# Optimization experiments

Measured on AMD Instinct MI355X. Metric: run time of the kernel, lower is better.

## Reference

```python
import jax, jax.numpy as jnp
import numpy as np

DIM = 256
HEADS = 8
DIM_HEAD = 64
INNER = HEADS * DIM_HEAD           # 512
DPG = DIM // HEADS                 # 32 in-channels per group (grouped conv)
EPS = 1e-5


def setup_inputs() -> dict:
    key = jax.random.key(0)
    ks = jax.random.split(key, 7)
    b, p, k = 4, 1024, 32
    x = jax.random.normal(ks[0], (b, p, k, DIM), dtype=jnp.float32)
    # BatchNorm2d affine params (torch default init: gamma=1, beta=0)
    bn_gamma = jnp.ones((DIM,), jnp.float32)
    bn_beta = jnp.zeros((DIM,), jnp.float32)
    # grouped 1x1 conv weights: per head maps DPG -> DIM_HEAD, shape [H, DIM_HEAD, DPG]
    Wq = jax.random.normal(ks[1], (HEADS, DIM_HEAD, DPG), jnp.float32) * 0.02
    Wk = jax.random.normal(ks[2], (HEADS, DIM_HEAD, DPG), jnp.float32) * 0.02
    Wv = jax.random.normal(ks[3], (HEADS, DIM_HEAD, DPG), jnp.float32) * 0.02
    # output Linear: y = x @ Wout + bout, Wout [INNER, DIM]
    Wout = jax.random.normal(ks[4], (INNER, DIM), jnp.float32) * 0.02
    bout = jnp.zeros((DIM,), jnp.float32)
    return {"x": x, "bn_gamma": bn_gamma, "bn_beta": bn_beta,
            "Wq": Wq, "Wk": Wk, "Wv": Wv, "Wout": Wout, "bout": bout}


def reference(x, bn_gamma, bn_beta, Wq, Wk, Wv, Wout, bout):
    b, p, k, d = x.shape
    scale = DIM_HEAD ** (-0.5)
    # BatchNorm2d in training mode: per-channel batch stats over (b, p, k)
    mean = jnp.mean(x, axis=(0, 1, 2))
    var = jnp.var(x, axis=(0, 1, 2))           # biased variance (torch BN normalization)
    xn = (x - mean) * jax.lax.rsqrt(var + EPS) * bn_gamma + bn_beta
    # grouped 1x1 conv projections: split channels into HEADS groups of DPG
    xg = xn.reshape(b, p, k, HEADS, DPG)       # [b,p,k,h,c]
    q = jnp.einsum('bpkhc,hoc->bphko', xg, Wq)  # [b,p,h,k,dim_head]
    kk = jnp.einsum('bpkhc,hoc->bphko', xg, Wk)
    v = jnp.einsum('bpkhc,hoc->bphko', xg, Wv)
    # attention over neighbors within each point
    dots = jnp.einsum('bphid,bphjd->bphij', q, kk) * scale  # [b,p,h,k,k]
    attn = jax.nn.softmax(dots, axis=-1)
    out = jnp.einsum('bphij,bphjd->bphid', attn, v)         # [b,p,h,k,dim_head]
    out = out.transpose(0, 1, 3, 2, 4).reshape(b, p, k, INNER)  # b p k (h d)
    return out @ Wout + bout                   # [b,p,k,dim]
```

## Files before the change

### kernel.cpp

```cpp
#include <hip/hip_runtime.h>

#define DIM    256
#define HEADS  8
#define DH     64
#define DPG    32
#define KNB    32
#define INNER  512
#define EPS    1e-5f

#define WS_SUM  0
#define WS_SSQ  256
#define WS_SC   512
#define WS_SH   768
#define WS_WF   1024
#define WS_QB   25600
#define WS_WT   27136

typedef float f32x4  __attribute__((ext_vector_type(4)));
typedef short bf16x8 __attribute__((ext_vector_type(8)));

__device__ __forceinline__ unsigned short f2bf(float f){
    unsigned u = __float_as_uint(f);
    u += 0x7fffu + ((u >> 16) & 1u);
    return (unsigned short)(u >> 16);
}
__device__ __forceinline__ unsigned packbf(float a, float b){
    return (unsigned)f2bf(a) | ((unsigned)f2bf(b) << 16);
}
__device__ __forceinline__ bf16x8 pack8(f32x4 a, f32x4 b){
    union { unsigned u[4]; bf16x8 v; } r;
    r.u[0] = packbf(a[0], a[1]); r.u[1] = packbf(a[2], a[3]);
    r.u[2] = packbf(b[0], b[1]); r.u[3] = packbf(b[2], b[3]);
    return r.v;
}

#define QKSWZ(row, col) ((row) * 64 + ((col) ^ ((((row) ^ ((row) >> 3)) & 7) << 3)))
#define VTSWZ(row, col) ((row) * 32 + ((col) ^ (((row) & 3) << 3)))

__global__ __launch_bounds__(256) void bn_stats_k(const f32x4* __restrict__ x4,
                                                  float* __restrict__ ws, int n4) {
    __shared__ f32x4 rs[4][64], rss[4][64];
    int tid = blockIdx.x * 256 + threadIdx.x;
    int stride = gridDim.x * 256;
    f32x4 s  = {0.f, 0.f, 0.f, 0.f};
    f32x4 ss = {0.f, 0.f, 0.f, 0.f};
    for (int f = tid; f < n4; f += stride) {
        f32x4 v = x4[f];
        s += v; ss += v * v;
    }
    int c4 = threadIdx.x & 63, wv = threadIdx.x >> 6;
    rs[wv][c4] = s; rss[wv][c4] = ss;
    __syncthreads();
    const float* rsf  = (const float*)rs;
    const float* rssf = (const float*)rss;
    int ch = threadIdx.x;
    float S = rsf[ch]  + rsf[256 + ch]  + rsf[512 + ch]  + rsf[768 + ch];
    float Q = rssf[ch] + rssf[256 + ch] + rssf[512 + ch] + rssf[768 + ch];
    atomicAdd(&ws[WS_SUM + ch], S);
    atomicAdd(&ws[WS_SSQ + ch], Q);
}

__global__ __launch_bounds__(256) void bn_finalize_k(const float* __restrict__ g,
                                                     const float* __restrict__ b,
                                                     float* __restrict__ ws, float inv_n) {
    int c = threadIdx.x;
    float mean = ws[WS_SUM + c] * inv_n;
    float var  = ws[WS_SSQ + c] * inv_n - mean * mean;
    float sc   = g[c] * rsqrtf(var + EPS);
    ws[WS_SC + c] = sc;
    ws[WS_SH + c] = b[c] - mean * sc;
}

__global__ __launch_bounds__(256) void wt_k(const float* __restrict__ Wout, float* __restrict__ ws) {
    __shared__ unsigned short tile[64][65];
    const int k0 = blockIdx.x * 64, n0 = blockIdx.y * 64;
    const int t = threadIdx.x;
    #pragma unroll
    for (int i = 0; i < 16; ++i) {
        int e = t + 256 * i;
        int kk = e >> 6, nn = e & 63;
        tile[kk][nn] = f2bf(Wout[(k0 + kk) * DIM + n0 + nn]);
    }
    __syncthreads();
    unsigned short* wt = (unsigned short*)(ws + WS_WT);
    #pragma unroll
    for (int i = 0; i < 2; ++i) {
        int f = t + 256 * i;
        int nn = f >> 3, kc = f & 7;
        union { unsigned short s[8]; uint4 u; } pk;
        #pragma unroll
        for (int j = 0; j < 8; ++j) pk.s[j] = tile[kc * 8 + j][nn];
        *(uint4*)(wt + (size_t)(n0 + nn) * INNER + k0 + kc * 8) = pk.u;
    }
}

__global__ __launch_bounds__(256) void fold_k(const float* __restrict__ Wq,
                                              const float* __restrict__ Wk,
                                              const float* __restrict__ Wv,
                                              float* __restrict__ ws) {
    __shared__ float wl[64][33];
    __shared__ float scs[DPG], shs[DPG];
    const int m = blockIdx.x, h = blockIdx.y, t = threadIdx.x;
    const float* W = (m == 0 ? Wq : (m == 1 ? Wk : Wv)) + h * DH * DPG;
    if (t < DPG) { scs[t] = ws[WS_SC + h * DPG + t]; shs[t] = ws[WS_SH + h * DPG + t]; }
    #pragma unroll
    for (int i = 0; i < 8; ++i) {
        int e = t + 256 * i;
        wl[e >> 5][e & 31] = W[e];
    }
    __syncthreads();
    const float qsc = (m == 0) ? 0.125f : 1.f;
    unsigned short* wf = (unsigned short*)(ws + WS_WF) + (m * HEADS + h) * DH * DPG;
    {
        int o = t >> 2, c0 = (t & 3) * 8;
        union { unsigned short s[8]; uint4 u; } pk;
        #pragma unroll
        for (int j = 0; j < 8; ++j) pk.s[j] = f2bf(wl[o][c0 + j] * scs[c0 + j] * qsc);
        *(uint4*)(wf + o * DPG + c0) = pk.u;
    }
    if (t < DH) {
        float bias = 0.f;
        #pragma unroll
        for (int c = 0; c < DPG; ++c) bias += shs[c] * wl[t][c];
        ws[WS_QB + (m * HEADS + h) * DH + t] = bias * qsc;
    }
}

__global__ __launch_bounds__(256, 3) void attn_fused(const float* __restrict__ x,
                                                     const float* __restrict__ ws,
                                                     const float* __restrict__ bout,
                                                     float* __restrict__ out) {
    __shared__ __align__(16) unsigned short lds[24576];

    const int t = threadIdx.x;
    const int w = t >> 6, L = t & 63;
    const int lr = L & 15, g = L >> 4;
    const long long rb = (long long)blockIdx.x * KNB;

    unsigned short* qsm = lds + w * 2048;
    unsigned short* ksm = lds + 8192 + w * 2048;
    unsigned short* vtm = lds + 16384 + w * 2048;
    unsigned short* psm = qsm;
    const unsigned short* wfb = (const unsigned short*)(ws + WS_WF);
    const unsigned short* WT  = (const unsigned short*)(ws + WS_WT);

    f32x4 av[2][2][4];

    #pragma unroll
    for (int hs = 0; hs < 2; ++hs) {
        const int h = w + hs * 4;

        bf16x8 xa[2];
        #pragma unroll
        for (int it = 0; it < 2; ++it) {
            const float* xp = x + (rb + it * 16 + lr) * DIM + h * DPG + g * 8;
            xa[it] = pack8(*(const f32x4*)xp, *(const f32x4*)(xp + 4));
        }

        #pragma unroll
        for (int m = 0; m < 3; ++m) {
            #pragma unroll
            for (int ot = 0; ot < 4; ++ot) {
                const int o = ot * 16 + lr;
                bf16x8 wf = *(const bf16x8*)(wfb + ((m * HEADS + h) * DH + o) * DPG + g * 8);
                float bv = ws[WS_QB + (m * HEADS + h) * DH + o];
                #pragma unroll
                for (int it = 0; it < 2; ++it) {
                    f32x4 c = {bv, bv, bv, bv};
                    c = __builtin_amdgcn_mfma_f32_16x16x32_bf16(xa[it], wf, c, 0, 0, 0);
                    if (m == 0) {
                        #pragma unroll
                        for (int r = 0; r < 4; ++r) {
                            int row = it * 16 + g * 4 + r;
                            qsm[QKSWZ(row, o)] = f2bf(c[r]);
                        }
                    } else if (m == 1) {
                        #pragma unroll
                        for (int r = 0; r < 4; ++r) {
                            int row = it * 16 + g * 4 + r;
                            ksm[QKSWZ(row, o)] = f2bf(c[r]);
                        }
                    } else {
                        uint2 u;
                        u.x = packbf(c[0], c[1]);
                        u.y = packbf(c[2], c[3]);
                        *(uint2*)(vtm + VTSWZ(o, it * 16 + g * 4)) = u;
                    }
                }
            }
        }

        f32x4 dt[2][2];
        #pragma unroll
        for (int it = 0; it < 2; ++it)
            #pragma unroll
            for (int jt = 0; jt < 2; ++jt) dt[it][jt] = (f32x4){0.f, 0.f, 0.f, 0.f};
        #pragma unroll
        for (int ksp = 0; ksp < 2; ++ksp) {
            bf16x8 qa[2], kb[2];
            #pragma unroll
            for (int it = 0; it < 2; ++it)
                qa[it] = *(const bf16x8*)(qsm + QKSWZ(it * 16 + lr, ksp * 32 + g * 8));
            #pragma unroll
            for (int jt = 0; jt < 2; ++jt)
                kb[jt] = *(const bf16x8*)(ksm + QKSWZ(jt * 16 + lr, ksp * 32 + g * 8));
            #pragma unroll
            for (int it = 0; it < 2; ++it)
                #pragma unroll
                for (int jt = 0; jt < 2; ++jt)
                    dt[it][jt] = __builtin_amdgcn_mfma_f32_16x16x32_bf16(qa[it], kb[jt], dt[it][jt], 0, 0, 0);
        }

        #pragma unroll
        for (int it = 0; it < 2; ++it)
            #pragma unroll
            for (int r = 0; r < 4; ++r) {
                float m0 = fmaxf(dt[it][0][r], dt[it][1][r]);
                m0 = fmaxf(m0, __shfl_xor(m0, 1, 64));
                m0 = fmaxf(m0, __shfl_xor(m0, 2, 64));
                m0 = fmaxf(m0, __shfl_xor(m0, 4, 64));
                m0 = fmaxf(m0, __shfl_xor(m0, 8, 64));
                float e0 = __expf(dt[it][0][r] - m0);
                float e1 = __expf(dt[it][1][r] - m0);
                float s = e0 + e1;
                s += __shfl_xor(s, 1, 64);
                s += __shfl_xor(s, 2, 64);
                s += __shfl_xor(s, 4, 64);
                s += __shfl_xor(s, 8, 64);
                float inv = 1.f / s;
                int row = it * 16 + g * 4 + r;
                psm[QKSWZ(row, lr)]      = f2bf(e0 * inv);
                psm[QKSWZ(row, lr + 16)] = f2bf(e1 * inv);
            }

        #pragma unroll
        for (int it = 0; it < 2; ++it) {
            bf16x8 pa = *(const bf16x8*)(psm + QKSWZ(it * 16 + lr, g * 8));
            #pragma unroll
            for (int ot = 0; ot < 4; ++ot) {
                bf16x8 vb = *(const bf16x8*)(vtm + VTSWZ(ot * 16 + lr, g * 8));
                f32x4 c = {0.f, 0.f, 0.f, 0.f};
                av[hs][it][ot] = __builtin_amdgcn_mfma_f32_16x16x32_bf16(pa, vb, c, 0, 0, 0);
            }
        }
    }

    __syncthreads();
    unsigned short* aos = lds;
    #pragma unroll
    for (int hs = 0; hs < 2; ++hs)
        #pragma unroll
        for (int it = 0; it < 2; ++it)
            #pragma unroll
            for (int ot = 0; ot < 4; ++ot)
                #pragma unroll
                for (int r = 0; r < 4; ++r)
                    aos[(it * 16 + g * 4 + r) * 520 + (w + hs * 4) * 64 + ot * 16 + lr]
                        = f2bf(av[hs][it][ot][r]);
    __syncthreads();

    f32x4 oacc[2][4];
    #pragma unroll
    for (int n4 = 0; n4 < 4; ++n4) {
        float bv = bout[(w * 4 + n4) * 16 + lr];
        oacc[0][n4] = (f32x4){bv, bv, bv, bv};
        oacc[1][n4] = (f32x4){bv, bv, bv, bv};
    }
    #pragma unroll 4
    for (int ksp = 0; ksp < 16; ++ksp) {
        bf16x8 a0 = *(const bf16x8*)(aos + lr * 520 + ksp * 32 + g * 8);
        bf16x8 a1 = *(const bf16x8*)(aos + (16 + lr) * 520 + ksp * 32 + g * 8);
        #pragma unroll
        for (int n4 = 0; n4 < 4; ++n4) {
            const int n = (w * 4 + n4) * 16 + lr;
            bf16x8 bvv = *(const bf16x8*)(WT + (size_t)n * INNER + ksp * 32 + g * 8);
            oacc[0][n4] = __builtin_amdgcn_mfma_f32_16x16x32_bf16(a0, bvv, oacc[0][n4], 0, 0, 0);
            oacc[1][n4] = __builtin_amdgcn_mfma_f32_16x16x32_bf16(a1, bvv, oacc[1][n4], 0, 0, 0);
        }
    }
    #pragma unroll
    for (int it = 0; it < 2; ++it)
        #pragma unroll
        for (int n4 = 0; n4 < 4; ++n4)
            #pragma unroll
            for (int r = 0; r < 4; ++r)
                out[(rb + it * 16 + g * 4 + r) * DIM + (w * 4 + n4) * 16 + lr] = oacc[it][n4][r];
}

extern "C" void kernel_launch(void* const* d_in, const int* in_sizes, int n_in,
                              void* d_out, int out_size, void* d_ws, size_t ws_size,
                              hipStream_t stream) {
    const float* x  = (const float*)d_in[0];
    const float* g  = (const float*)d_in[1];
    const float* b  = (const float*)d_in[2];
    const float* wq = (const float*)d_in[3];
    const float* wk = (const float*)d_in[4];
    const float* wv = (const float*)d_in[5];
    const float* wo = (const float*)d_in[6];
    const float* bo = (const float*)d_in[7];
    float* ws = (float*)d_ws;

    int rows = in_sizes[0] / DIM;
    int npts = rows / KNB;

    hipMemsetAsync(d_ws, 0, 2048, stream);
    bn_stats_k<<<512, 256, 0, stream>>>((const f32x4*)x, ws, rows * (DIM / 4));
    bn_finalize_k<<<1, 256, 0, stream>>>(g, b, ws, 1.0f / (float)rows);
    wt_k<<<dim3(INNER / 64, DIM / 64), 256, 0, stream>>>(wo, ws);
    fold_k<<<dim3(3, HEADS), 256, 0, stream>>>(wq, wk, wv, ws);
    attn_fused<<<npts, 256, 0, stream>>>(x, ws, bo, (float*)d_out);
}
```

Measured before the change: 428.4 us.

## Cut attention LDS footprint to raise occupancy, merge BN finalize into fold

The fused attention kernel now computes V only after the softmax and stores it in the K buffer, which shrinks shared memory from 48KB to 32KB and lets the launch bounds target 5 blocks per SM instead of 3. The padded output staging layout is replaced by an XOR swizzle, and bf16 packing uses the paired conversion intrinsic. The BN stats kernel unrolls its loads 4x, doubles its grid and spreads atomics over 4 banks to reduce contention. The separate finalize kernel is folded into fold_k to save a launch. The risks are register spilling under the tighter launch bound and longer live ranges for the x fragments.

```diff
diff --git a/kernel.cpp b/kernel.cpp
--- a/kernel.cpp
+++ b/kernel.cpp
@@ -1,4 +1,5 @@
 #include <hip/hip_runtime.h>
+#include <hip/hip_bf16.h>
 
 #define DIM    256
 #define HEADS  8
@@ -8,13 +9,11 @@
 #define INNER  512
 #define EPS    1e-5f
 
-#define WS_SUM  0
-#define WS_SSQ  256
-#define WS_SC   512
-#define WS_SH   768
-#define WS_WF   1024
-#define WS_QB   25600
-#define WS_WT   27136
+#define WS_SUMB 0
+#define WS_SSQB 1024
+#define WS_WF   2048
+#define WS_QB   26624
+#define WS_WT   28160
 
 typedef float f32x4  __attribute__((ext_vector_type(4)));
 typedef short bf16x8 __attribute__((ext_vector_type(8)));
@@ -25,7 +24,9 @@
     return (unsigned short)(u >> 16);
 }
 __device__ __forceinline__ unsigned packbf(float a, float b){
-    return (unsigned)f2bf(a) | ((unsigned)f2bf(b) << 16);
+    union { __hip_bfloat162 h; unsigned u; } c;
+    c.h = __float22bfloat162_rn(make_float2(a, b));
+    return c.u;
 }
 __device__ __forceinline__ bf16x8 pack8(f32x4 a, f32x4 b){
     union { unsigned u[4]; bf16x8 v; } r;
@@ -34,20 +35,30 @@
     return r.v;
 }
 
-#define QKSWZ(row, col) ((row) * 64 + ((col) ^ ((((row) ^ ((row) >> 3)) & 7) << 3)))
-#define VTSWZ(row, col) ((row) * 32 + ((col) ^ (((row) & 3) << 3)))
+#define QKSWZ(row, col) ((row) * 64 + ((col) ^ ((((row) ^ ((row) >> 2)) & 7) << 3)))
+#define AOSWZ(row, col) ((row) * 512 + ((col) ^ (((row) & 7) << 3)))
 
 __global__ __launch_bounds__(256) void bn_stats_k(const f32x4* __restrict__ x4,
                                                   float* __restrict__ ws, int n4) {
     __shared__ f32x4 rs[4][64], rss[4][64];
-    int tid = blockIdx.x * 256 + threadIdx.x;
-    int stride = gridDim.x * 256;
+    const int tid = blockIdx.x * 256 + threadIdx.x;
+    const int stride = gridDim.x * 256;
     f32x4 s  = {0.f, 0.f, 0.f, 0.f};
     f32x4 ss = {0.f, 0.f, 0.f, 0.f};
-    for (int f = tid; f < n4; f += stride) {
-        f32x4 v = x4[f];
-        s += v; ss += v * v;
-    }
+    int f = tid;
+    const int nloop = n4 / (4 * stride);
+    for (int i = 0; i < nloop; ++i) {
+        f32x4 v0 = x4[f];
+        f32x4 v1 = x4[f + stride];
+        f32x4 v2 = x4[f + 2 * stride];
+        f32x4 v3 = x4[f + 3 * stride];
+        f += 4 * stride;
+        s += v0; ss += v0 * v0;
+        s += v1; ss += v1 * v1;
+        s += v2; ss += v2 * v2;
+        s += v3; ss += v3 * v3;
+    }
+    for (; f < n4; f += stride) { f32x4 v = x4[f]; s += v; ss += v * v; }
     int c4 = threadIdx.x & 63, wv = threadIdx.x >> 6;
     rs[wv][c4] = s; rss[wv][c4] = ss;
     __syncthreads();
@@ -56,19 +67,9 @@
     int ch = threadIdx.x;
     float S = rsf[ch]  + rsf[256 + ch]  + rsf[512 + ch]  + rsf[768 + ch];
     float Q = rssf[ch] + rssf[256 + ch] + rssf[512 + ch] + rssf[768 + ch];
-    atomicAdd(&ws[WS_SUM + ch], S);
-    atomicAdd(&ws[WS_SSQ + ch], Q);
-}
-
-__global__ __launch_bounds__(256) void bn_finalize_k(const float* __restrict__ g,
-                                                     const float* __restrict__ b,
-                                                     float* __restrict__ ws, float inv_n) {
-    int c = threadIdx.x;
-    float mean = ws[WS_SUM + c] * inv_n;
-    float var  = ws[WS_SSQ + c] * inv_n - mean * mean;
-    float sc   = g[c] * rsqrtf(var + EPS);
-    ws[WS_SC + c] = sc;
-    ws[WS_SH + c] = b[c] - mean * sc;
+    int bank = (blockIdx.x & 3) * 256;
+    atomicAdd(&ws[WS_SUMB + bank + ch], S);
+    atomicAdd(&ws[WS_SSQB + bank + ch], Q);
 }
 
 __global__ __launch_bounds__(256) void wt_k(const float* __restrict__ Wout, float* __restrict__ ws) {
@@ -97,12 +98,23 @@
 __global__ __launch_bounds__(256) void fold_k(const float* __restrict__ Wq,
                                               const float* __restrict__ Wk,
                                               const float* __restrict__ Wv,
-                                              float* __restrict__ ws) {
+                                              const float* __restrict__ gam,
+                                              const float* __restrict__ bet,
+                                              float* __restrict__ ws, float inv_n) {
     __shared__ float wl[64][33];
     __shared__ float scs[DPG], shs[DPG];
     const int m = blockIdx.x, h = blockIdx.y, t = threadIdx.x;
     const float* W = (m == 0 ? Wq : (m == 1 ? Wk : Wv)) + h * DH * DPG;
-    if (t < DPG) { scs[t] = ws[WS_SC + h * DPG + t]; shs[t] = ws[WS_SH + h * DPG + t]; }
+    if (t < DPG) {
+        int c = h * DPG + t;
+        float S = ws[WS_SUMB + c] + ws[WS_SUMB + 256 + c] + ws[WS_SUMB + 512 + c] + ws[WS_SUMB + 768 + c];
+        float Q = ws[WS_SSQB + c] + ws[WS_SSQB + 256 + c] + ws[WS_SSQB + 512 + c] + ws[WS_SSQB + 768 + c];
+        float mean = S * inv_n;
+        float var  = Q * inv_n - mean * mean;
+        float sc   = gam[c] * rsqrtf(var + EPS);
+        scs[t] = sc;
+        shs[t] = bet[c] - mean * sc;
+    }
     #pragma unroll
     for (int i = 0; i < 8; ++i) {
         int e = t + 256 * i;
@@ -126,11 +138,11 @@
     }
 }
 
-__global__ __launch_bounds__(256, 3) void attn_fused(const float* __restrict__ x,
+__global__ __launch_bounds__(256, 5) void attn_fused(const float* __restrict__ x,
                                                      const float* __restrict__ ws,
                                                      const float* __restrict__ bout,
                                                      float* __restrict__ out) {
-    __shared__ __align__(16) unsigned short lds[24576];
+    __shared__ __align__(16) unsigned short lds[16384];
 
     const int t = threadIdx.x;
     const int w = t >> 6, L = t & 63;
@@ -139,26 +151,29 @@
 
     unsigned short* qsm = lds + w * 2048;
     unsigned short* ksm = lds + 8192 + w * 2048;
-    unsigned short* vtm = lds + 16384 + w * 2048;
     unsigned short* psm = qsm;
+    unsigned short* vtm = ksm;
     const unsigned short* wfb = (const unsigned short*)(ws + WS_WF);
     const unsigned short* WT  = (const unsigned short*)(ws + WS_WT);
 
+    bf16x8 xa[2][2];
+    #pragma unroll
+    for (int hs = 0; hs < 2; ++hs)
+        #pragma unroll
+        for (int it = 0; it < 2; ++it) {
+            const float* xp = x + (rb + it * 16 + lr) * DIM + (w + hs * 4) * DPG + g * 8;
+            xa[hs][it] = pack8(*(const f32x4*)xp, *(const f32x4*)(xp + 4));
+        }
+
     f32x4 av[2][2][4];
 
     #pragma unroll
     for (int hs = 0; hs < 2; ++hs) {
         const int h = w + hs * 4;
 
-        bf16x8 xa[2];
-        #pragma unroll
-        for (int it = 0; it < 2; ++it) {
-            const float* xp = x + (rb + it * 16 + lr) * DIM + h * DPG + g * 8;
-            xa[it] = pack8(*(const f32x4*)xp, *(const f32x4*)(xp + 4));
-        }
-
-        #pragma unroll
-        for (int m = 0; m < 3; ++m) {
+        #pragma unroll
+        for (int m = 0; m < 2; ++m) {
+            unsigned short* dst = m ? ksm : qsm;
             #pragma unroll
             for (int ot = 0; ot < 4; ++ot) {
                 const int o = ot * 16 + lr;
@@ -167,25 +182,14 @@
                 #pragma unroll
                 for (int it = 0; it < 2; ++it) {
                     f32x4 c = {bv, bv, bv, bv};
-                    c = __builtin_amdgcn_mfma_f32_16x16x32_bf16(xa[it], wf, c, 0, 0, 0);
-                    if (m == 0) {
-                        #pragma unroll
-                        for (int r = 0; r < 4; ++r) {
-                            int row = it * 16 + g * 4 + r;
-                            qsm[QKSWZ(row, o)] = f2bf(c[r]);
-                        }
-                    } else if (m == 1) {
-                        #pragma unroll
-                        for (int r = 0; r < 4; ++r) {
-                            int row = it * 16 + g * 4 + r;
-                            ksm[QKSWZ(row, o)] = f2bf(c[r]);
-                        }
-                    } else {
-                        uint2 u;
-                        u.x = packbf(c[0], c[1]);
-                        u.y = packbf(c[2], c[3]);
-                        *(uint2*)(vtm + VTSWZ(o, it * 16 + g * 4)) = u;
-                    }
+                    c = __builtin_amdgcn_mfma_f32_16x16x32_bf16(xa[hs][it], wf, c, 0, 0, 0);
+                    unsigned u01 = packbf(c[0], c[1]);
+                    unsigned u23 = packbf(c[2], c[3]);
+                    const int r0 = it * 16 + g * 4;
+                    dst[QKSWZ(r0 + 0, o)] = (unsigned short)u01;
+                    dst[QKSWZ(r0 + 1, o)] = (unsigned short)(u01 >> 16);
+                    dst[QKSWZ(r0 + 2, o)] = (unsigned short)u23;
+                    dst[QKSWZ(r0 + 3, o)] = (unsigned short)(u23 >> 16);
                 }
             }
         }
@@ -229,16 +233,33 @@
                 s += __shfl_xor(s, 8, 64);
                 float inv = 1.f / s;
                 int row = it * 16 + g * 4 + r;
-                psm[QKSWZ(row, lr)]      = f2bf(e0 * inv);
-                psm[QKSWZ(row, lr + 16)] = f2bf(e1 * inv);
+                unsigned up = packbf(e0 * inv, e1 * inv);
+                psm[QKSWZ(row, lr)]      = (unsigned short)up;
+                psm[QKSWZ(row, lr + 16)] = (unsigned short)(up >> 16);
             }
+
+        #pragma unroll
+        for (int ot = 0; ot < 4; ++ot) {
+            const int o = ot * 16 + lr;
+            bf16x8 wf = *(const bf16x8*)(wfb + ((2 * HEADS + h) * DH + o) * DPG + g * 8);
+            float bv = ws[WS_QB + (2 * HEADS + h) * DH + o];
+            #pragma unroll
+            for (int it = 0; it < 2; ++it) {
+                f32x4 c = {bv, bv, bv, bv};
+                c = __builtin_amdgcn_mfma_f32_16x16x32_bf16(xa[hs][it], wf, c, 0, 0, 0);
+                uint2 u;
+                u.x = packbf(c[0], c[1]);
+                u.y = packbf(c[2], c[3]);
+                *(uint2*)(vtm + QKSWZ(o & 31, (o >> 5) * 32 + it * 16 + g * 4)) = u;
+            }
+        }
 
         #pragma unroll
         for (int it = 0; it < 2; ++it) {
             bf16x8 pa = *(const bf16x8*)(psm + QKSWZ(it * 16 + lr, g * 8));
             #pragma unroll
             for (int ot = 0; ot < 4; ++ot) {
-                bf16x8 vb = *(const bf16x8*)(vtm + VTSWZ(ot * 16 + lr, g * 8));
+                bf16x8 vb = *(const bf16x8*)(vtm + QKSWZ((ot & 1) * 16 + lr, (ot >> 1) * 32 + g * 8));
                 f32x4 c = {0.f, 0.f, 0.f, 0.f};
                 av[hs][it][ot] = __builtin_amdgcn_mfma_f32_16x16x32_bf16(pa, vb, c, 0, 0, 0);
             }
@@ -255,7 +276,7 @@
             for (int ot = 0; ot < 4; ++ot)
                 #pragma unroll
                 for (int r = 0; r < 4; ++r)
-                    aos[(it * 16 + g * 4 + r) * 520 + (w + hs * 4) * 64 + ot * 16 + lr]
+                    aos[AOSWZ(it * 16 + g * 4 + r, (w + hs * 4) * 64 + ot * 16 + lr)]
                         = f2bf(av[hs][it][ot][r]);
     __syncthreads();
 
@@ -268,8 +289,8 @@
     }
     #pragma unroll 4
     for (int ksp = 0; ksp < 16; ++ksp) {
-        bf16x8 a0 = *(const bf16x8*)(aos + lr * 520 + ksp * 32 + g * 8);
-        bf16x8 a1 = *(const bf16x8*)(aos + (16 + lr) * 520 + ksp * 32 + g * 8);
+        bf16x8 a0 = *(const bf16x8*)(aos + AOSWZ(lr, ksp * 32 + g * 8));
+        bf16x8 a1 = *(const bf16x8*)(aos + AOSWZ(16 + lr, ksp * 32 + g * 8));
         #pragma unroll
         for (int n4 = 0; n4 < 4; ++n4) {
             const int n = (w * 4 + n4) * 16 + lr;
@@ -303,10 +324,9 @@
     int rows = in_sizes[0] / DIM;
     int npts = rows / KNB;
 
-    hipMemsetAsync(d_ws, 0, 2048, stream);
-    bn_stats_k<<<512, 256, 0, stream>>>((const f32x4*)x, ws, rows * (DIM / 4));
-    bn_finalize_k<<<1, 256, 0, stream>>>(g, b, ws, 1.0f / (float)rows);
+    hipMemsetAsync(d_ws, 0, 8192, stream);
     wt_k<<<dim3(INNER / 64, DIM / 64), 256, 0, stream>>>(wo, ws);
-    fold_k<<<dim3(3, HEADS), 256, 0, stream>>>(wq, wk, wv, ws);
+    bn_stats_k<<<1024, 256, 0, stream>>>((const f32x4*)x, ws, rows * (DIM / 4));
+    fold_k<<<dim3(3, HEADS), 256, 0, stream>>>(wq, wk, wv, g, b, ws, 1.0f / (float)rows);
     attn_fused<<<npts, 256, 0, stream>>>(x, ws, bo, (float*)d_out);
 }
```

After: 482.0 us. 12.5% more time.
